# Kernel tuning notes

Measured on AMD Instinct MI355X. Metric: run time of the kernel, lower is better.

## Reference

```python
import jax, jax.numpy as jnp
import numpy as np

D = 512      # d_model
H = 8        # heads
DK = D // H  # 64
DFF = 2048
EPS = 1e-6


def layer_norm(x, gamma, beta):
    # Faithful to the module: std uses Bessel correction (torch default unbiased)
    # and eps is added to std (not variance); gamma/beta are scalars init to 1.
    m = jnp.mean(x, axis=-1, keepdims=True)
    var = jnp.sum((x - m) ** 2, axis=-1, keepdims=True) / (x.shape[-1] - 1)
    return gamma * (x - m) / (jnp.sqrt(var) + EPS) + beta


def setup_inputs() -> dict:
    key = jax.random.key(0)
    ks = jax.random.split(key, 12)
    s = 0.02
    inp = {
        "x": jax.random.normal(ks[0], (4, 2048, D), dtype=jnp.float32),
        "src_mask": jnp.ones((4, 1, 1, 2048), dtype=jnp.int32),
        "Wq": jax.random.normal(ks[1], (D, D), jnp.float32) * s,
        "bq": jnp.zeros((D,), jnp.float32),
        "Wk": jax.random.normal(ks[2], (D, D), jnp.float32) * s,
        "bk": jnp.zeros((D,), jnp.float32),
        "Wv": jax.random.normal(ks[3], (D, D), jnp.float32) * s,
        "bv": jnp.zeros((D,), jnp.float32),
        "Wo": jax.random.normal(ks[4], (D, D), jnp.float32) * s,
        "bo": jnp.zeros((D,), jnp.float32),
        "W1": jax.random.normal(ks[5], (D, DFF), jnp.float32) * s,
        "b1": jnp.zeros((DFF,), jnp.float32),
        "W2": jax.random.normal(ks[6], (DFF, D), jnp.float32) * s,
        "b2": jnp.zeros((D,), jnp.float32),
        "g1": jnp.ones((), jnp.float32),
        "be1": jnp.ones((), jnp.float32),
        "g2": jnp.ones((), jnp.float32),
        "be2": jnp.ones((), jnp.float32),
    }
    return inp


def reference(x, src_mask, Wq, bq, Wk, bk, Wv, bv, Wo, bo,
              W1, b1, W2, b2, g1, be1, g2, be2):
    B, S, _ = x.shape

    # --- residual 1: pre-LN self-attention ---
    xn = layer_norm(x, g1, be1)                               # [B,S,D]
    q = (xn @ Wq + bq).reshape(B, S, H, DK).transpose(0, 2, 1, 3)  # [B,H,S,DK]
    k = (xn @ Wk + bk).reshape(B, S, H, DK).transpose(0, 2, 1, 3)
    v = (xn @ Wv + bv).reshape(B, S, H, DK).transpose(0, 2, 1, 3)

    scores = jnp.einsum('bhqd,bhkd->bhqk', q, k) / np.float32(np.sqrt(DK))
    scores = jnp.where(src_mask == 0, jnp.float32(-1e9), scores)  # [B,H,S,S]
    attn = jax.nn.softmax(scores, axis=-1)
    o = jnp.einsum('bhqk,bhkd->bhqd', attn, v)                # [B,H,S,DK]
    o = o.transpose(0, 2, 1, 3).reshape(B, S, D)
    x = x + (o @ Wo + bo)

    # --- residual 2: pre-LN feed-forward ---
    xn = layer_norm(x, g2, be2)
    ff = jax.nn.relu(xn @ W1 + b1) @ W2 + b2
    return x + ff
```

## Files before the change

kernel.cpp:

```cpp
#include <hip/hip_runtime.h>
#include <hip/hip_bf16.h>


#define B_   4
#define S_   2048
#define D_   512
#define H_   8
#define DK_  64
#define DFF_ 2048
#define M_   (B_*S_)

typedef __attribute__((ext_vector_type(8))) short short8;
typedef __attribute__((ext_vector_type(4))) float f32x4;
typedef __attribute__((ext_vector_type(16))) float f32x16;

#define QSCALE 0.18033688011f

#if __has_builtin(__builtin_amdgcn_exp2f)
#define EXP2(x) __builtin_amdgcn_exp2f(x)
#else
#define EXP2(x) exp2f(x)
#endif

#define GLOAD_LDS(gp, lp) __builtin_amdgcn_global_load_lds( \
    (const __attribute__((address_space(1))) void*)(gp),    \
    (__attribute__((address_space(3))) void*)(lp), 16, 0, 0)

#define WAITV(N) asm volatile("s_waitcnt vmcnt(" #N ")" ::: "memory")
#define BARRIER() __builtin_amdgcn_s_barrier()

__device__ inline unsigned short f2bf(float f) {
    union { float f; unsigned u; } v; v.f = f;
    unsigned r = v.u + 0x7fffu + ((v.u >> 16) & 1u);
    return (unsigned short)(r >> 16);
}

__device__ inline unsigned cvtpk_bf16(float a, float b) {
    unsigned r;
    asm("v_cvt_pk_bf16_f32 %0, %1, %2" : "=v"(r) : "v"(a), "v"(b));
    return r;
}

__device__ inline void permswap32(unsigned &x, unsigned &y) {
    asm volatile("v_permlane32_swap_b32 %0, %1" : "+v"(x), "+v"(y));
}

__global__ __launch_bounds__(256) void transT_kernel(
    const float* __restrict__ Wq, const float* __restrict__ Wk,
    const float* __restrict__ Wv, const float* __restrict__ Wo,
    const float* __restrict__ W1, const float* __restrict__ W2,
    const float* __restrict__ bq, const float* __restrict__ bk,
    const float* __restrict__ bv, const int* __restrict__ mask,
    float* __restrict__ qkvb, unsigned* __restrict__ mbits,
    short* __restrict__ dst,
    const float* __restrict__ x, const float* __restrict__ g1,
    const float* __restrict__ be1, short* __restrict__ xn) {
    const int id = blockIdx.x, t = threadIdx.x;
    if (id >= 769) {
        int w = t >> 6, l = t & 63;
        int row = (id - 769) * 4 + w;
        const float4* xr = (const float4*)(x + (size_t)row * D_);
        float4 a = xr[l * 2], b = xr[l * 2 + 1];
        float s = a.x + a.y + a.z + a.w + b.x + b.y + b.z + b.w;
        for (int off = 32; off > 0; off >>= 1) s += __shfl_xor(s, off);
        float mean = s * (1.f / 512.f);
        float e[8] = {a.x - mean, a.y - mean, a.z - mean, a.w - mean,
                      b.x - mean, b.y - mean, b.z - mean, b.w - mean};
        float vs = 0.f;
        #pragma unroll
        for (int i = 0; i < 8; i++) vs += e[i] * e[i];
        for (int off = 32; off > 0; off >>= 1) vs += __shfl_xor(vs, off);
        float scale = g1[0] / (sqrtf(vs * (1.f / 511.f)) + 1e-6f);
        float b0 = be1[0];
        union { short8 v; short s[8]; } o;
        #pragma unroll
        for (int i = 0; i < 8; i++) o.s[i] = (short)f2bf(e[i] * scale + b0);
        *(short8*)(xn + (size_t)row * D_ + l * 8) = o.v;
        return;
    }
    if (id == 768) {
        for (int i = t; i < 1536; i += 256)
            qkvb[i] = (i < 512) ? bq[i] * QSCALE : (i < 1024) ? bk[i - 512] : bv[i - 1024];
        if (t < 128) {
            int b = t >> 5, tile = t & 31;
            const int* mr = mask + b * S_ + tile * 64;
            bool all1 = true;
            for (int u = 0; u < 64; u++) all1 &= (mr[u] != 0);
            unsigned long long bal = __ballot(all1);
            if ((t & 63) == 0) {
                mbits[(t >> 6) * 2]     = (unsigned)bal;
                mbits[(t >> 6) * 2 + 1] = (unsigned)(bal >> 32);
            }
        }
        return;
    }
    __shared__ float T[64][65];
    const float* src; short* d; int K, N, tk, tn;
    if (id < 256) {
        int m = id >> 6;
        src = (m == 0) ? Wq : (m == 1) ? Wk : (m == 2) ? Wv : Wo;
        d = dst + (size_t)m * 512 * 512; K = 512; N = 512;
        int j = id & 63; tk = j >> 3; tn = j & 7;
    } else if (id < 512) {
        src = W1; d = dst + (size_t)4 * 512 * 512; K = 512; N = 2048;
        int j = id - 256; tk = j >> 5; tn = j & 31;
    } else {
        src = W2; d = dst + (size_t)4 * 512 * 512 + 2048 * 512; K = 2048; N = 512;
        int j = id - 512; tk = j >> 3; tn = j & 7;
    }
    const int k0 = tk * 64, n0 = tn * 64;
    #pragma unroll
    for (int i = 0; i < 4; i++) {
        int r = i * 16 + (t >> 4), c4 = (t & 15) * 4;
        float4 v = *(const float4*)(src + (size_t)(k0 + r) * N + n0 + c4);
        T[r][c4] = v.x; T[r][c4 + 1] = v.y; T[r][c4 + 2] = v.z; T[r][c4 + 3] = v.w;
    }
    __syncthreads();
    #pragma unroll
    for (int p = 0; p < 2; p++) {
        int j = p * 256 + t, n = j >> 3, kc = (j & 7) * 8;
        union { short8 v; short s[8]; } o;
        #pragma unroll
        for (int u = 0; u < 8; u++) o.s[u] = (short)f2bf(T[kc + u][n]);
        *(short8*)(d + (size_t)(n0 + n) * K + k0 + kc) = o.v;
    }
}

__global__ __launch_bounds__(256) void ln_kernel(const float* __restrict__ x,
                                                 const float* __restrict__ g,
                                                 const float* __restrict__ be,
                                                 short* __restrict__ out) {
    int w = threadIdx.x >> 6, l = threadIdx.x & 63;
    int row = blockIdx.x * 4 + w;
    const float4* xr = (const float4*)(x + (size_t)row * D_);
    float4 a = xr[l * 2], b = xr[l * 2 + 1];
    float s = a.x + a.y + a.z + a.w + b.x + b.y + b.z + b.w;
    for (int off = 32; off > 0; off >>= 1) s += __shfl_xor(s, off);
    float mean = s * (1.f / 512.f);
    float e[8] = {a.x - mean, a.y - mean, a.z - mean, a.w - mean,
                  b.x - mean, b.y - mean, b.z - mean, b.w - mean};
    float vs = 0.f;
    #pragma unroll
    for (int i = 0; i < 8; i++) vs += e[i] * e[i];
    for (int off = 32; off > 0; off >>= 1) vs += __shfl_xor(vs, off);
    float scale = g[0] / (sqrtf(vs * (1.f / 511.f)) + 1e-6f);
    float b0 = be[0];
    union { short8 v; short s[8]; } o;
    #pragma unroll
    for (int i = 0; i < 8; i++) o.s[i] = (short)f2bf(e[i] * scale + b0);
    *(short8*)(out + (size_t)row * D_ + l * 8) = o.v;
}

template <int BN, int MODE>
__global__ __launch_bounds__(256, 2) void gemm_kernel(
    const short* __restrict__ A, const short* __restrict__ Bt,
    const float* __restrict__ bias, const float* __restrict__ resid,
    void* __restrict__ out, int M, int N, int K) {
    constexpr int NF = BN / 32;
    __shared__ __align__(16) short smem[2 * 128 * 64 + 2 * BN * 64];
    auto As = [&](int b) -> short* { return smem + b * 8192; };
    auto Bs = [&](int b) -> short* { return smem + 16384 + b * BN * 64; };
    const int t = threadIdx.x;
    const int w = t >> 6, l = t & 63;
    const int wm = w >> 1, wn = w & 1;
    const int lr = l & 15, lk = l >> 4;
    const int m0 = blockIdx.x * 128, n0 = blockIdx.y * BN;
    f32x4 acc[4][NF] = {};

    auto stage = [&](int buf, int k0) {
        #pragma unroll
        for (int p = 0; p < 4; p++) {
            int id = p * 256 + t;
            int r = id >> 3, c = id & 7, cs = c ^ (r & 7);
            GLOAD_LDS(A + (size_t)(m0 + r) * K + k0 + cs * 8, As(buf) + (p * 256 + w * 64) * 8);
        }
        #pragma unroll
        for (int p = 0; p < BN / 32; p++) {
            int id = p * 256 + t;
            int r = id >> 3, c = id & 7, cs = c ^ (r & 7);
            GLOAD_LDS(Bt + (size_t)(n0 + r) * K + k0 + cs * 8, Bs(buf) + (p * 256 + w * 64) * 8);
        }
    };

    const int nk = K >> 6;
    stage(0, 0);

    for (int tk = 0; tk < nk; ++tk) {
        const int cur = tk & 1;
        if (tk + 1 < nk) {
            stage(cur ^ 1, (tk + 1) * 64);
            if constexpr (BN == 128) WAITV(8); else WAITV(6);
        } else WAITV(0);
        BARRIER();
        short8 af[4][2], bf[NF][2];
        #pragma unroll
        for (int f = 0; f < 4; f++) {
            int ra = wm * 64 + f * 16 + lr;
            #pragma unroll
            for (int kk = 0; kk < 2; kk++)
                af[f][kk] = *(const short8*)&As(cur)[ra * 64 + (((kk * 4 + lk) ^ (ra & 7)) << 3)];
        }
        #pragma unroll
        for (int f = 0; f < NF; f++) {
            int rb = wn * (BN / 2) + f * 16 + lr;
            #pragma unroll
            for (int kk = 0; kk < 2; kk++)
                bf[f][kk] = *(const short8*)&Bs(cur)[rb * 64 + (((kk * 4 + lk) ^ (rb & 7)) << 3)];
        }
        __builtin_amdgcn_s_setprio(1);
        #pragma unroll
        for (int kk = 0; kk < 2; kk++)
            #pragma unroll
            for (int mf = 0; mf < 4; mf++)
                #pragma unroll
                for (int nf = 0; nf < NF; nf++)
                    acc[mf][nf] = __builtin_amdgcn_mfma_f32_16x16x32_bf16(
                        af[mf][kk], bf[nf][kk], acc[mf][nf], 0, 0, 0);
        __builtin_amdgcn_s_setprio(0);
        BARRIER();
    }

    if constexpr (MODE == 0) {
        const int seg = n0 >> 9;
        #pragma unroll
        for (int mf = 0; mf < 4; mf++) {
            #pragma unroll
            for (int nf = 0; nf < NF; nf++) {
                int mb = m0 + wm * 64 + mf * 16 + lk * 4;
                int n  = n0 + wn * (BN / 2) + nf * 16 + lr;
                float bv = bias[n];
                int bb = mb >> 11, sl = mb & 2047, nl = n & 511;
                unsigned short* ob = (unsigned short*)out + (size_t)seg * M_ * D_;
                float v[4];
                #pragma unroll
                for (int i = 0; i < 4; i++) {
                    float val = acc[mf][nf][i];
                    if (seg == 0) val *= QSCALE;
                    v[i] = val + bv;
                }
                if (seg < 2) {
                    #pragma unroll
                    for (int i = 0; i < 4; i++)
                        ob[(((size_t)(bb * 8 + (nl >> 6)) * 2048 + sl + i) << 6) + (nl & 63)] = f2bf(v[i]);
                } else {
                    uint2 pk;
                    pk.x = cvtpk_bf16(v[0], v[1]);
                    pk.y = cvtpk_bf16(v[2], v[3]);
                    *(uint2*)&ob[(((size_t)(bb * 8 + (nl >> 6)) * 64 + (nl & 63)) << 11) + sl] = pk;
                }
            }
        }
    } else if constexpr (MODE == 1) {
        float* E = (float*)smem;
        #pragma unroll
        for (int mf = 0; mf < 4; mf++)
            #pragma unroll
            for (int nf = 0; nf < NF; nf++) {
                int n_loc = wn * (BN / 2) + nf * 16 + lr;
                float bv = bias[n0 + n_loc];
                int c = n_loc >> 4;
                #pragma unroll
                for (int i = 0; i < 4; i++) {
                    int m_loc = wm * 64 + mf * 16 + lk * 4 + i;
                    E[m_loc * 64 + ((c ^ (m_loc & 3)) << 4) + (n_loc & 15)] =
                        acc[mf][nf][i] + bv;
                }
            }
        BARRIER();
        #pragma unroll
        for (int pass = 0; pass < 8; pass++) {
            int fid = pass * 256 + t;
            int row = fid >> 4, c4 = fid & 15;
            int lc = c4 >> 2, j = c4 & 3;
            f32x4 v = *(f32x4*)&E[row * 64 + (((lc ^ (row & 3))) << 4) + j * 4];
            int m = m0 + row, n = n0 + lc * 16 + j * 4;
            f32x4 rv = *(const f32x4*)&resid[(size_t)m * N + n];
            *(f32x4*)&((float*)out)[(size_t)m * N + n] = v + rv;
        }
    } else {
        unsigned short* E16 = (unsigned short*)smem;
        #pragma unroll
        for (int mf = 0; mf < 4; mf++)
            #pragma unroll
            for (int nf = 0; nf < NF; nf++) {
                int n_loc = wn * (BN / 2) + nf * 16 + lr;
                float bv = bias[n0 + n_loc];
                int c = n_loc >> 3;
                #pragma unroll
                for (int i = 0; i < 4; i++) {
                    int m_loc = wm * 64 + mf * 16 + lk * 4 + i;
                    E16[m_loc * 128 + ((c ^ (m_loc & 7)) << 3) + (n_loc & 7)] =
                        f2bf(fmaxf(acc[mf][nf][i] + bv, 0.f));
                }
            }
        BARRIER();
        #pragma unroll
        for (int pass = 0; pass < 8; pass++) {
            int fid = pass * 256 + t;
            int row = fid >> 4, c = fid & 15;
            short8 v = *(short8*)&E16[row * 128 + ((c ^ (row & 7)) << 3)];
            *(short8*)&((unsigned short*)out)[(size_t)(m0 + row) * N + n0 + c * 8] = v;
        }
    }
}

__global__ __launch_bounds__(512, 2) void attn_kernel(
    const short* __restrict__ Q, const short* __restrict__ Kb,
    const short* __restrict__ Vt, const int* __restrict__ mask,
    const unsigned* __restrict__ mbits, unsigned short* __restrict__ O) {
    __shared__ __align__(16) short sm[24576];
    const int t = threadIdx.x, w = t >> 6, l = t & 63;
    const int ql = l & 31, hi = l >> 5;
    const int wh = w >> 2, wl = w & 3;
    const int bh = blockIdx.x, b = bh >> 3, h = bh & 7;
    const int q0 = blockIdx.y * 256 + wl * 64;

    short8 qf[2][4];
    #pragma unroll
    for (int qs = 0; qs < 2; qs++) {
        const short* qrow = Q + ((size_t)bh * S_ + q0 + qs * 32 + ql) * DK_;
        #pragma unroll
        for (int s = 0; s < 4; s++) qf[qs][s] = *(const short8*)(qrow + s * 16 + hi * 8);
    }

    const short* kg = Kb + (size_t)bh * S_ * DK_;
    const short* vg = Vt + (size_t)bh * DK_ * S_;
    const int* mrow = mask + b * S_;
    const unsigned mb = mbits[b];

    short* KH = sm + wh * 12288;
    short* kdw = KH + wl * 512;

    const int kro = wl * 8 + (l >> 3);
    const int kc = (l & 7) ^ (kro & 7);
    const short* kp = kg + ((size_t)(wh * 1024 + kro)) * 64 + kc * 8;
    const int vr = kro, vc = (l & 7) ^ (vr & 7);
    const int vdk = vr + 32 * (vc >> 2), vkvo = (vc & 3) * 8;
    const short* vp = vg + (size_t)vdk * 2048 + vkvo + wh * 1024;

    auto stage = [&](int buf) {
        GLOAD_LDS(kp, kdw + buf * 4096);
        GLOAD_LDS(vp, kdw + buf * 4096 + 2048);
        kp += 32 * 64;
        vp += 32;
    };

    f32x16 o_acc[2][2] = {};
    float la[2][4] = {};

    stage(0); stage(1);
    WAITV(2);
    BARRIER();

    for (int tt = 0; tt < 32; ++tt) {
        const int cur = tt % 3;
        const int gt = wh * 32 + tt;
        if (tt + 2 < 32) stage((tt + 2) % 3);
        const short* Ks = KH + cur * 4096;
        const short* Vs = Ks + 2048;

        short8 kf[4];
        #pragma unroll
        for (int s = 0; s < 4; s++)
            kf[s] = *(const short8*)&Ks[ql * 64 + (((s * 2 + hi) ^ (ql & 7)) << 3)];
        f32x16 sa = {}, sb = {};
        __builtin_amdgcn_s_setprio(1);
        #pragma unroll
        for (int s = 0; s < 4; s++)
            sa = __builtin_amdgcn_mfma_f32_32x32x16_bf16(kf[s], qf[0][s], sa, 0, 0, 0);
        #pragma unroll
        for (int s = 0; s < 4; s++)
            sb = __builtin_amdgcn_mfma_f32_32x32x16_bf16(kf[s], qf[1][s], sb, 0, 0, 0);
        __builtin_amdgcn_s_setprio(0);

        if (!((mb >> (gt >> 1)) & 1)) {
            #pragma unroll
            for (int r = 0; r < 16; r++) {
                int k = gt * 32 + (r & 3) + 8 * (r >> 2) + 4 * hi;
                if (mrow[k] == 0) { sa[r] = -1.4426950e9f; sb[r] = -1.4426950e9f; }
            }
        }

        unsigned Dp[2][8];
        {
            float p[16];
            #pragma unroll
            for (int r = 0; r < 16; r++) { p[r] = EXP2(sa[r]); la[0][r & 3] += p[r]; }
            #pragma unroll
            for (int j = 0; j < 8; j++) Dp[0][j] = cvtpk_bf16(p[2 * j], p[2 * j + 1]);
            #pragma unroll
            for (int r = 0; r < 16; r++) { p[r] = EXP2(sb[r]); la[1][r & 3] += p[r]; }
            #pragma unroll
            for (int j = 0; j < 8; j++) Dp[1][j] = cvtpk_bf16(p[2 * j], p[2 * j + 1]);
        }

        #pragma unroll
        for (int s16 = 0; s16 < 2; s16++) {
            union { unsigned u[4]; short8 v; } pu[2];
            #pragma unroll
            for (int qs = 0; qs < 2; qs++) {
                unsigned f0 = Dp[qs][s16 * 4 + 0], f1 = Dp[qs][s16 * 4 + 1];
                unsigned f2 = Dp[qs][s16 * 4 + 2], f3 = Dp[qs][s16 * 4 + 3];
                permswap32(f0, f2);
                permswap32(f1, f3);
                pu[qs].u[0] = f0; pu[qs].u[1] = f1; pu[qs].u[2] = f2; pu[qs].u[3] = f3;
            }
            __builtin_amdgcn_s_setprio(1);
            #pragma unroll
            for (int dt = 0; dt < 2; dt++) {
                short8 vf = *(const short8*)&Vs[ql * 64 + (((dt * 4 + s16 * 2 + hi) ^ (ql & 7)) << 3)];
                o_acc[0][dt] = __builtin_amdgcn_mfma_f32_32x32x16_bf16(vf, pu[0].v, o_acc[0][dt], 0, 0, 0);
                o_acc[1][dt] = __builtin_amdgcn_mfma_f32_32x32x16_bf16(vf, pu[1].v, o_acc[1][dt], 0, 0, 0);
            }
            __builtin_amdgcn_s_setprio(0);
        }

        if (tt < 30) WAITV(2); else WAITV(0);
        BARRIER();
    }

    float lp[2];
    #pragma unroll
    for (int qs = 0; qs < 2; qs++) {
        float s = (la[qs][0] + la[qs][1]) + (la[qs][2] + la[qs][3]);
        lp[qs] = s + __shfl_xor(s, 32);
    }

    float* C = (float*)sm;
    f32x4* Cv = (f32x4*)sm;
    #pragma unroll
    for (int qs = 0; qs < 2; qs++) {
        __syncthreads();
        if (wh == 1) {
            #pragma unroll
            for (int j = 0; j < 8; j++) {
                f32x4 v;
                #pragma unroll
                for (int e = 0; e < 4; e++) v[e] = o_acc[qs][j >> 2][(j & 3) * 4 + e];
                Cv[wl * 512 + j * 64 + l] = v;
            }
            C[8192 + wl * 64 + l] = lp[qs];
        }
        __syncthreads();
        if (wh == 0) {
            #pragma unroll
            for (int j = 0; j < 8; j++) {
                f32x4 v = Cv[wl * 512 + j * 64 + l];
                #pragma unroll
                for (int e = 0; e < 4; e++) o_acc[qs][j >> 2][(j & 3) * 4 + e] += v[e];
            }
            float linv = 1.f / (lp[qs] + C[8192 + wl * 64 + l]);
            unsigned short* orow = O + ((size_t)b * S_ + q0 + qs * 32 + ql) * D_ + h * 64;
            #pragma unroll
            for (int dt = 0; dt < 2; dt++)
                #pragma unroll
                for (int g = 0; g < 4; g++) {
                    unsigned u0 = cvtpk_bf16(o_acc[qs][dt][g * 4 + 0] * linv, o_acc[qs][dt][g * 4 + 1] * linv);
                    unsigned u1 = cvtpk_bf16(o_acc[qs][dt][g * 4 + 2] * linv, o_acc[qs][dt][g * 4 + 3] * linv);
                    uint2 pk; pk.x = u0; pk.y = u1;
                    *(uint2*)(orow + dt * 32 + 8 * g + 4 * hi) = pk;
                }
        }
    }
}

extern "C" void kernel_launch(void* const* d_in, const int* in_sizes, int n_in,
                              void* d_out, int out_size, void* d_ws, size_t ws_size,
                              hipStream_t stream) {
    const float* x    = (const float*)d_in[0];
    const int*   mask = (const int*)d_in[1];
    const float* Wq = (const float*)d_in[2];  const float* bq  = (const float*)d_in[3];
    const float* Wk = (const float*)d_in[4];  const float* bk  = (const float*)d_in[5];
    const float* Wv = (const float*)d_in[6];  const float* bv  = (const float*)d_in[7];
    const float* Wo = (const float*)d_in[8];  const float* bo  = (const float*)d_in[9];
    const float* W1 = (const float*)d_in[10]; const float* b1  = (const float*)d_in[11];
    const float* W2 = (const float*)d_in[12]; const float* b2  = (const float*)d_in[13];
    const float* g1 = (const float*)d_in[14]; const float* be1 = (const float*)d_in[15];
    const float* g2 = (const float*)d_in[16]; const float* be2 = (const float*)d_in[17];

    short* WqT = (short*)d_ws;
    short* W1T = WqT + 4 * 512 * 512;
    short* W2T = W1T + 2048 * 512;
    short* xn  = W2T + 512 * 2048;
    short* Qb  = xn  + (size_t)M_ * D_;
    short* Kbf = Qb  + (size_t)M_ * D_;
    short* Vtb = Kbf + (size_t)M_ * D_;
    short* Ob  = Vtb + (size_t)M_ * D_;
    float* x2  = (float*)(Ob + (size_t)M_ * D_);
    float* qkvb = x2;
    unsigned* mbits = (unsigned*)(qkvb + 1536);
    short* WoT = WqT + 3 * 512 * 512;
    short* Hb  = Qb;

    transT_kernel<<<769 + M_ / 4, 256, 0, stream>>>(Wq, Wk, Wv, Wo, W1, W2,
                                                    bq, bk, bv, mask, qkvb, mbits, WqT,
                                                    x, g1, be1, xn);

    gemm_kernel<128, 0><<<dim3(64, 12), 256, 0, stream>>>(xn, WqT, qkvb, nullptr,
                                                          Qb, M_, 1536, 512);

    attn_kernel<<<dim3(B_ * H_, S_ / 256), 512, 0, stream>>>(Qb, Kbf, Vtb, mask, mbits,
                                                             (unsigned short*)Ob);

    gemm_kernel<64, 1><<<dim3(64, 8), 256, 0, stream>>>(Ob, WoT, bo, x, x2, M_, 512, 512);

    ln_kernel<<<M_ / 4, 256, 0, stream>>>(x2, g2, be2, xn);

    gemm_kernel<128, 2><<<dim3(64, 16), 256, 0, stream>>>(xn, W1T, b1, nullptr, Hb, M_, 2048, 512);
    gemm_kernel<64, 1><<<dim3(64, 8), 256, 0, stream>>>(Hb, W2T, b2, x2, (float*)d_out, M_, 512, 2048);
}
```

Before: 138.5 us.

## Split attention KV range four ways per block with double-buffered loads

The attention kernel is re-partitioned so each 512-thread block handles 128 queries (two query warps) across four KV-range groups instead of 256 queries across two KV halves. The grid doubles, giving more blocks to fill the CUs, and the triple-buffered K/V pipeline becomes a double buffer with a wait-and-barrier at the top of each iteration. The cost is a larger cross-warp reduction of partial outputs and row sums at the end, 64KB of LDS per block, and K/V tiles being loaded twice as many times overall.

```diff
diff --git a/kernel.cpp b/kernel.cpp
--- a/kernel.cpp
+++ b/kernel.cpp
@@ -308,12 +308,12 @@
     const short* __restrict__ Q, const short* __restrict__ Kb,
     const short* __restrict__ Vt, const int* __restrict__ mask,
     const unsigned* __restrict__ mbits, unsigned short* __restrict__ O) {
-    __shared__ __align__(16) short sm[24576];
+    __shared__ __align__(16) short sm[32768];
     const int t = threadIdx.x, w = t >> 6, l = t & 63;
     const int ql = l & 31, hi = l >> 5;
-    const int wh = w >> 2, wl = w & 3;
+    const int wk = w >> 1, wq = w & 1;
     const int bh = blockIdx.x, b = bh >> 3, h = bh & 7;
-    const int q0 = blockIdx.y * 256 + wl * 64;
+    const int q0 = blockIdx.y * 128 + wq * 64;
 
     short8 qf[2][4];
     #pragma unroll
@@ -328,34 +328,42 @@
     const int* mrow = mask + b * S_;
     const unsigned mb = mbits[b];
 
-    short* KH = sm + wh * 12288;
-    short* kdw = KH + wl * 512;
-
-    const int kro = wl * 8 + (l >> 3);
-    const int kc = (l & 7) ^ (kro & 7);
-    const short* kp = kg + ((size_t)(wh * 1024 + kro)) * 64 + kc * 8;
-    const int vr = kro, vc = (l & 7) ^ (vr & 7);
-    const int vdk = vr + 32 * (vc >> 2), vkvo = (vc & 3) * 8;
-    const short* vp = vg + (size_t)vdk * 2048 + vkvo + wh * 1024;
+    short* KH = sm + wk * 8192;
+    const int ldsoff = wq * 1024;
+
+    const short* kp[2];
+    const short* vp[2];
+    #pragma unroll
+    for (int p = 0; p < 2; p++) {
+        int r = wq * 16 + p * 8 + (l >> 3);
+        int c = l & 7, cs = c ^ (r & 7);
+        kp[p] = kg + ((size_t)(wk * 512 + r)) * 64 + cs * 8;
+        int vdk = r + 32 * (cs >> 2), kvo = (cs & 3) * 8;
+        vp[p] = vg + (size_t)vdk * 2048 + wk * 512 + kvo;
+    }
 
     auto stage = [&](int buf) {
-        GLOAD_LDS(kp, kdw + buf * 4096);
-        GLOAD_LDS(vp, kdw + buf * 4096 + 2048);
-        kp += 32 * 64;
-        vp += 32;
+        short* Kd = KH + buf * 4096 + ldsoff;
+        #pragma unroll
+        for (int p = 0; p < 2; p++) {
+            GLOAD_LDS(kp[p], Kd + p * 512);
+            GLOAD_LDS(vp[p], Kd + 2048 + p * 512);
+            kp[p] += 32 * 64;
+            vp[p] += 32;
+        }
     };
 
     f32x16 o_acc[2][2] = {};
     float la[2][4] = {};
 
-    stage(0); stage(1);
-    WAITV(2);
-    BARRIER();
-
-    for (int tt = 0; tt < 32; ++tt) {
-        const int cur = tt % 3;
-        const int gt = wh * 32 + tt;
-        if (tt + 2 < 32) stage((tt + 2) % 3);
+    stage(0);
+
+    for (int tt = 0; tt < 16; ++tt) {
+        const int cur = tt & 1;
+        const int gt = wk * 16 + tt;
+        if (tt + 1 < 16) { stage(cur ^ 1); WAITV(4); }
+        else WAITV(0);
+        BARRIER();
         const short* Ks = KH + cur * 4096;
         const short* Vs = Ks + 2048;
 
@@ -415,7 +423,6 @@
             __builtin_amdgcn_s_setprio(0);
         }
 
-        if (tt < 30) WAITV(2); else WAITV(0);
         BARRIER();
     }
 
@@ -431,25 +438,32 @@
     #pragma unroll
     for (int qs = 0; qs < 2; qs++) {
         __syncthreads();
-        if (wh == 1) {
+        if (wk > 0) {
+            int base = ((wk - 1) * 2 + wq) * 512;
             #pragma unroll
             for (int j = 0; j < 8; j++) {
                 f32x4 v;
                 #pragma unroll
                 for (int e = 0; e < 4; e++) v[e] = o_acc[qs][j >> 2][(j & 3) * 4 + e];
-                Cv[wl * 512 + j * 64 + l] = v;
-            }
-            C[8192 + wl * 64 + l] = lp[qs];
+                Cv[base + j * 64 + l] = v;
+            }
+            C[12288 + ((wk - 1) * 2 + wq) * 64 + l] = lp[qs];
         }
         __syncthreads();
-        if (wh == 0) {
-            #pragma unroll
-            for (int j = 0; j < 8; j++) {
-                f32x4 v = Cv[wl * 512 + j * 64 + l];
-                #pragma unroll
-                for (int e = 0; e < 4; e++) o_acc[qs][j >> 2][(j & 3) * 4 + e] += v[e];
-            }
-            float linv = 1.f / (lp[qs] + C[8192 + wl * 64 + l]);
+        if (wk == 0) {
+            float lsum = lp[qs];
+            #pragma unroll
+            for (int g = 0; g < 3; g++) {
+                int base = (g * 2 + wq) * 512;
+                #pragma unroll
+                for (int j = 0; j < 8; j++) {
+                    f32x4 v = Cv[base + j * 64 + l];
+                    #pragma unroll
+                    for (int e = 0; e < 4; e++) o_acc[qs][j >> 2][(j & 3) * 4 + e] += v[e];
+                }
+                lsum += C[12288 + (g * 2 + wq) * 64 + l];
+            }
+            float linv = 1.f / lsum;
             unsigned short* orow = O + ((size_t)b * S_ + q0 + qs * 32 + ql) * D_ + h * 64;
             #pragma unroll
             for (int dt = 0; dt < 2; dt++)
@@ -499,7 +513,7 @@
     gemm_kernel<128, 0><<<dim3(64, 12), 256, 0, stream>>>(xn, WqT, qkvb, nullptr,
                                                           Qb, M_, 1536, 512);
 
-    attn_kernel<<<dim3(B_ * H_, S_ / 256), 512, 0, stream>>>(Qb, Kbf, Vtb, mask, mbits,
+    attn_kernel<<<dim3(B_ * H_, S_ / 128), 512, 0, stream>>>(Qb, Kbf, Vtb, mask, mbits,
                                                              (unsigned short*)Ob);
 
     gemm_kernel<64, 1><<<dim3(64, 8), 256, 0, stream>>>(Ob, WoT, bo, x, x2, M_, 512, 512);
```

Measured after the change: 146.4 us. +5.7%, slower.
